# Optimization experiments

Measured on AMD Instinct MI355X. Metric: run time of the kernel, lower is better.

## Reference

```python
import jax, jax.numpy as jnp
import numpy as np


def setup_inputs() -> dict:
    key = jax.random.key(0)
    k1, k2, k3 = jax.random.split(key, 3)
    x = jax.random.normal(k1, (8, 3, 256, 256), dtype=jnp.float32)
    conv_w = jax.random.normal(k2, (64, 3), dtype=jnp.float32)  # 1x1 conv weight [O, C]
    w = jax.random.normal(k3, (64, 8), dtype=jnp.float32)       # per-channel LBP weights
    return {"x": x, "conv_w": conv_w, "w": w}


def _heaviside(d):
    # torch.heaviside(d, 0.): 1 where d > 0, else 0 (including d == 0)
    return jnp.where(d > 0, jnp.ones((), d.dtype), jnp.zeros((), d.dtype))


def reference(x, conv_w, w):
    # 1x1 conv, no bias: [N,C,H,W] x [O,C] -> [N,O,H,W]
    y = jnp.einsum('nchw,oc->nohw', x, conv_w)
    c = y[:, :, 1:-1, 1:-1]  # center, [N,O,H-2,W-2]
    # 8 neighbor shifts in the original order
    shifts = [
        y[:, :, 0:-2, 0:-2], y[:, :, 0:-2, 1:-1], y[:, :, 0:-2, 2:],
        y[:, :, 1:-1, 0:-2], y[:, :, 2:, 0:-2], y[:, :, 2:, 1:-1],
        y[:, :, 2:, 2:],    y[:, :, 1:-1, 2:],
    ]
    act = jnp.stack([_heaviside(c - s) for s in shifts], axis=2)  # [N,O,8,H-2,W-2]
    # weighted reduction over the 8 directions with exp(w)
    x_cat = jnp.einsum('nolhw,ol->nohw', act, jnp.exp(w))
    padded = jnp.pad(x_cat, ((0, 0), (0, 0), (1, 1), (1, 1)))  # ZeroPad2d(1)
    # res=True: concat raw input along channels -> [N, 3+O, H, W]
    return jnp.concatenate([x, padded], axis=1)
```

## Files before the change

### kernel.cpp

```cpp
#include <hip/hip_runtime.h>


__device__ __forceinline__ float wave_shr1(float v) {
    return __int_as_float(
        __builtin_amdgcn_update_dpp(0, __float_as_int(v), 0x138, 0xf, 0xf, false));
}
__device__ __forceinline__ float wave_shl1(float v) {
    return __int_as_float(
        __builtin_amdgcn_update_dpp(0, __float_as_int(v), 0x130, 0xf, 0xf, false));
}

__global__ __launch_bounds__(256) void lbp_all(
    const float* __restrict__ x,
    const float* __restrict__ conv_w,
    const float* __restrict__ w,
    float* __restrict__ out)
{
#pragma clang fp contract(off)
    const int n    = blockIdx.z;
    const int og   = blockIdx.y;
    const int tid  = threadIdx.x;
    const int lane = tid & 63;
    const int wv   = tid >> 6;
    const int col  = lane * 4;
    const int R    = blockIdx.x * 8;
    const int hrow0 = R + wv * 2;

    __shared__ float xt[3][10][256];
    __shared__ float ews[128];

    if (tid < 128) ews[tid] = expf(w[og * 128 + tid]);

    const float* xn = x + (size_t)n * 3 * 65536;

    for (int f = tid; f < 1920; f += 256) {
        const int ch = f / 640;
        const int rr = (f - ch * 640) >> 6;
        const int l4 = f & 63;
        int gr = R - 1 + rr;
        gr = gr < 0 ? 0 : (gr > 255 ? 255 : gr);
        *(float4*)&xt[ch][rr][l4 * 4] =
            *(const float4*)(xn + (size_t)ch * 65536 + (size_t)gr * 256 + l4 * 4);
    }
    __syncthreads();

    if (og == 0) {
        #pragma unroll
        for (int ch = 0; ch < 3; ++ch) {
            float* cp = out + ((((size_t)n * 67 + ch) * 256 + hrow0) * 256 + col);
            *(float4*)cp         = *(const float4*)&xt[ch][2 * wv + 1][col];
            *(float4*)(cp + 256) = *(const float4*)&xt[ch][2 * wv + 2][col];
        }
    }

    float* obase = out + ((((size_t)n * 67 + 3 + og * 16) * 256 + hrow0) * 256 + col);

    #pragma unroll 1
    for (int oi = 0; oi < 16; ++oi) {
        const int o = og * 16 + oi;
        const float cw0 = conv_w[o * 3 + 0];
        const float cw1 = conv_w[o * 3 + 1];
        const float cw2 = conv_w[o * 3 + 2];

        const float e0 = ews[oi * 8 + 0], e1 = ews[oi * 8 + 1];
        const float e2 = ews[oi * 8 + 2], e3 = ews[oi * 8 + 3];
        const float e4 = ews[oi * 8 + 4], e5 = ews[oi * 8 + 5];
        const float e6 = ews[oi * 8 + 6], e7 = ews[oi * 8 + 7];

        float Y[4][6];
        #pragma unroll
        for (int r = 0; r < 4; ++r) {
            const int lr = 2 * wv + r;
            const float4 a = *(const float4*)&xt[0][lr][col];
            const float4 b = *(const float4*)&xt[1][lr][col];
            const float4 c = *(const float4*)&xt[2][lr][col];
            float4 yv;
            yv.x = a.x * cw0 + b.x * cw1 + c.x * cw2;
            yv.y = a.y * cw0 + b.y * cw1 + c.y * cw2;
            yv.z = a.z * cw0 + b.z * cw1 + c.z * cw2;
            yv.w = a.w * cw0 + b.w * cw1 + c.w * cw2;
            Y[r][1] = yv.x; Y[r][2] = yv.y; Y[r][3] = yv.z; Y[r][4] = yv.w;
            Y[r][0] = wave_shr1(yv.w);
            Y[r][5] = wave_shl1(yv.x);
        }

        #pragma unroll
        for (int k = 0; k < 2; ++k) {
            const int hrow = hrow0 + k;
            float res[4];
            if (hrow == 0 || hrow == 255) {
                res[0] = res[1] = res[2] = res[3] = 0.f;
            } else {
                const float* up  = Y[k];
                const float* mid = Y[k + 1];
                const float* dn  = Y[k + 2];
                #pragma unroll
                for (int j = 0; j < 4; ++j) {
                    const float c = mid[j + 1];
                    const float n0 = (c > up [j    ]) ? e0 : 0.f;
                    const float n1 = (c > up [j + 1]) ? e1 : 0.f;
                    const float n2 = (c > up [j + 2]) ? e2 : 0.f;
                    const float n3 = (c > mid[j    ]) ? e3 : 0.f;
                    const float n4 = (c > dn [j    ]) ? e4 : 0.f;
                    const float n5 = (c > dn [j + 1]) ? e5 : 0.f;
                    const float n6 = (c > dn [j + 2]) ? e6 : 0.f;
                    const float n7 = (c > mid[j + 2]) ? e7 : 0.f;
                    res[j] = ((n0 + n1) + (n2 + n3)) + ((n4 + n5) + (n6 + n7));
                }
                if (lane == 0)  res[0] = 0.f;
                if (lane == 63) res[3] = 0.f;
            }
            *(float4*)(obase + (size_t)oi * 65536 + (size_t)k * 256) =
                make_float4(res[0], res[1], res[2], res[3]);
        }
    }
}

extern "C" void kernel_launch(void* const* d_in, const int* in_sizes, int n_in,
                              void* d_out, int out_size, void* d_ws, size_t ws_size,
                              hipStream_t stream) {
    const float* x      = (const float*)d_in[0];
    const float* conv_w = (const float*)d_in[1];
    const float* w      = (const float*)d_in[2];
    float* out          = (float*)d_out;

    dim3 grid(32, 4, 8);
    dim3 block(256);
    hipLaunchKernelGGL(lbp_all, grid, block, 0, stream, x, conv_w, w, out);
}
```

Baseline: 154.2 us.

## Assign one output channel per wave and stream rows through a rolling register window

Work is remapped so each wave owns one output channel over a 16-row strip, instead of looping over 16 channels for 2 rows. The 1x1 conv result is kept in a rotating 4-row register window, so only one new row is computed per output row. This cuts the redundant conv recomputation from halo rows and moves the exp(w) weights into per-wave scalar registers. Blocks become 1024 threads with a taller shared tile, which may lower occupancy. The 8-term sum is now accumulated sequentially rather than as a tree, which changes float rounding slightly.

```diff
diff --git a/kernel.cpp b/kernel.cpp
--- a/kernel.cpp
+++ b/kernel.cpp
@@ -10,7 +10,7 @@
         __builtin_amdgcn_update_dpp(0, __float_as_int(v), 0x130, 0xf, 0xf, false));
 }
 
-__global__ __launch_bounds__(256) void lbp_all(
+__global__ __launch_bounds__(1024) void lbp_all(
     const float* __restrict__ x,
     const float* __restrict__ conv_w,
     const float* __restrict__ w,
@@ -23,97 +23,104 @@
     const int lane = tid & 63;
     const int wv   = tid >> 6;
     const int col  = lane * 4;
-    const int R    = blockIdx.x * 8;
-    const int hrow0 = R + wv * 2;
+    const int s    = blockIdx.x * 16;
+    const int c    = og * 16 + wv;
 
-    __shared__ float xt[3][10][256];
-    __shared__ float ews[128];
-
-    if (tid < 128) ews[tid] = expf(w[og * 128 + tid]);
+    __shared__ float xt[3][18][256];
 
     const float* xn = x + (size_t)n * 3 * 65536;
 
-    for (int f = tid; f < 1920; f += 256) {
-        const int ch = f / 640;
-        const int rr = (f - ch * 640) >> 6;
-        const int l4 = f & 63;
-        int gr = R - 1 + rr;
+    for (int f = tid; f < 3456; f += 1024) {
+        const int ch  = f / 1152;
+        const int rem = f - ch * 1152;
+        const int rr  = rem >> 6;
+        const int l4  = rem & 63;
+        int gr = s - 1 + rr;
         gr = gr < 0 ? 0 : (gr > 255 ? 255 : gr);
         *(float4*)&xt[ch][rr][l4 * 4] =
             *(const float4*)(xn + (size_t)ch * 65536 + (size_t)gr * 256 + l4 * 4);
     }
+
+    const float cw0 = conv_w[c * 3 + 0];
+    const float cw1 = conv_w[c * 3 + 1];
+    const float cw2 = conv_w[c * 3 + 2];
+    float ee[8];
+    #pragma unroll
+    for (int i = 0; i < 8; ++i)
+        ee[i] = __uint_as_float(__builtin_amdgcn_readfirstlane(
+                    __float_as_uint(expf(w[c * 8 + i]))));
+    const float e0 = ee[0], e1 = ee[1], e2 = ee[2], e3 = ee[3];
+    const float e4 = ee[4], e5 = ee[5], e6 = ee[6], e7 = ee[7];
+
     __syncthreads();
 
-    if (og == 0) {
-        #pragma unroll
-        for (int ch = 0; ch < 3; ++ch) {
-            float* cp = out + ((((size_t)n * 67 + ch) * 256 + hrow0) * 256 + col);
-            *(float4*)cp         = *(const float4*)&xt[ch][2 * wv + 1][col];
-            *(float4*)(cp + 256) = *(const float4*)&xt[ch][2 * wv + 2][col];
-        }
+    if (og == 0 && wv < 3) {
+        float* cp = out + ((((size_t)n * 67 + wv) * 256 + s) * 256 + col);
+        #pragma unroll 4
+        for (int r = 0; r < 16; ++r)
+            *(float4*)(cp + (size_t)r * 256) = *(const float4*)&xt[wv][r + 1][col];
     }
 
-    float* obase = out + ((((size_t)n * 67 + 3 + og * 16) * 256 + hrow0) * 256 + col);
+    float* ob = out + ((((size_t)n * 67 + 3 + c) * 256 + s) * 256 + col);
 
-    #pragma unroll 1
-    for (int oi = 0; oi < 16; ++oi) {
-        const int o = og * 16 + oi;
-        const float cw0 = conv_w[o * 3 + 0];
-        const float cw1 = conv_w[o * 3 + 1];
-        const float cw2 = conv_w[o * 3 + 2];
+    float Y[4][6];
 
-        const float e0 = ews[oi * 8 + 0], e1 = ews[oi * 8 + 1];
-        const float e2 = ews[oi * 8 + 2], e3 = ews[oi * 8 + 3];
-        const float e4 = ews[oi * 8 + 4], e5 = ews[oi * 8 + 5];
-        const float e6 = ews[oi * 8 + 6], e7 = ews[oi * 8 + 7];
+#define CONV(SLOT, IDX) do {                                                  \
+        const float4 a  = *(const float4*)&xt[0][(IDX)][col];                 \
+        const float4 b  = *(const float4*)&xt[1][(IDX)][col];                 \
+        const float4 cc = *(const float4*)&xt[2][(IDX)][col];                 \
+        float4 yv;                                                            \
+        yv.x = a.x * cw0 + b.x * cw1 + cc.x * cw2;                            \
+        yv.y = a.y * cw0 + b.y * cw1 + cc.y * cw2;                            \
+        yv.z = a.z * cw0 + b.z * cw1 + cc.z * cw2;                            \
+        yv.w = a.w * cw0 + b.w * cw1 + cc.w * cw2;                            \
+        Y[SLOT][1] = yv.x; Y[SLOT][2] = yv.y;                                 \
+        Y[SLOT][3] = yv.z; Y[SLOT][4] = yv.w;                                 \
+        Y[SLOT][0] = wave_shr1(yv.w);                                         \
+        Y[SLOT][5] = wave_shl1(yv.x);                                         \
+    } while (0)
 
-        float Y[4][6];
-        #pragma unroll
-        for (int r = 0; r < 4; ++r) {
-            const int lr = 2 * wv + r;
-            const float4 a = *(const float4*)&xt[0][lr][col];
-            const float4 b = *(const float4*)&xt[1][lr][col];
-            const float4 c = *(const float4*)&xt[2][lr][col];
-            float4 yv;
-            yv.x = a.x * cw0 + b.x * cw1 + c.x * cw2;
-            yv.y = a.y * cw0 + b.y * cw1 + c.y * cw2;
-            yv.z = a.z * cw0 + b.z * cw1 + c.z * cw2;
-            yv.w = a.w * cw0 + b.w * cw1 + c.w * cw2;
-            Y[r][1] = yv.x; Y[r][2] = yv.y; Y[r][3] = yv.z; Y[r][4] = yv.w;
-            Y[r][0] = wave_shr1(yv.w);
-            Y[r][5] = wave_shl1(yv.x);
-        }
+    CONV(3, 0);
+    CONV(0, 1);
 
-        #pragma unroll
-        for (int k = 0; k < 2; ++k) {
-            const int hrow = hrow0 + k;
-            float res[4];
-            if (hrow == 0 || hrow == 255) {
-                res[0] = res[1] = res[2] = res[3] = 0.f;
-            } else {
-                const float* up  = Y[k];
-                const float* mid = Y[k + 1];
-                const float* dn  = Y[k + 2];
-                #pragma unroll
-                for (int j = 0; j < 4; ++j) {
-                    const float c = mid[j + 1];
-                    const float n0 = (c > up [j    ]) ? e0 : 0.f;
-                    const float n1 = (c > up [j + 1]) ? e1 : 0.f;
-                    const float n2 = (c > up [j + 2]) ? e2 : 0.f;
-                    const float n3 = (c > mid[j    ]) ? e3 : 0.f;
-                    const float n4 = (c > dn [j    ]) ? e4 : 0.f;
-                    const float n5 = (c > dn [j + 1]) ? e5 : 0.f;
-                    const float n6 = (c > dn [j + 2]) ? e6 : 0.f;
-                    const float n7 = (c > mid[j + 2]) ? e7 : 0.f;
-                    res[j] = ((n0 + n1) + (n2 + n3)) + ((n4 + n5) + (n6 + n7));
-                }
-                if (lane == 0)  res[0] = 0.f;
-                if (lane == 63) res[3] = 0.f;
-            }
-            *(float4*)(obase + (size_t)oi * 65536 + (size_t)k * 256) =
-                make_float4(res[0], res[1], res[2], res[3]);
-        }
+#define STEP(JI) do {                                                         \
+    const int j = jq + (JI);                                                  \
+    const int r = s + j;                                                      \
+    CONV(((JI) + 1) & 3, j + 2);                                  \
+    const float* up  = Y[((JI) + 3) & 3];                         \
+    const float* mid = Y[(JI) & 3];                               \
+    const float* dn  = Y[((JI) + 1) & 3];                         \
+    float res[4];                                                             \
+    if (r == 0 || r == 255) {                               \
+        res[0] = res[1] = res[2] = res[3] = 0.f;                              \
+    } else {                                                                  \
+        _Pragma("unroll")                                                     \
+        for (int jj = 0; jj < 4; ++jj) {                                      \
+            const float cv = mid[jj + 1];                                     \
+            float acc;                                                        \
+            acc  = (cv > up [jj    ]) ? e0 : 0.f;                \
+            acc += (cv > up [jj + 1]) ? e1 : 0.f;                \
+            acc += (cv > up [jj + 2]) ? e2 : 0.f;                \
+            acc += (cv > mid[jj    ]) ? e3 : 0.f;                \
+            acc += (cv > dn [jj    ]) ? e4 : 0.f;                \
+            acc += (cv > dn [jj + 1]) ? e5 : 0.f;                \
+            acc += (cv > dn [jj + 2]) ? e6 : 0.f;                \
+            acc += (cv > mid[jj + 2]) ? e7 : 0.f;                \
+            res[jj] = acc;                                                    \
+        }                                                                     \
+        if (lane == 0)  res[0] = 0.f;                            \
+        if (lane == 63) res[3] = 0.f;                            \
+    }                                                                         \
+    *(float4*)(ob + (size_t)j * 256) =                                        \
+        make_float4(res[0], res[1], res[2], res[3]);                          \
+} while (0)
+
+    #pragma unroll
+    for (int jq = 0; jq < 16; jq += 4) {
+        STEP(0); STEP(1); STEP(2); STEP(3);
     }
+#undef STEP
+#undef CONV
 }
 
 extern "C" void kernel_launch(void* const* d_in, const int* in_sizes, int n_in,
@@ -124,7 +131,7 @@
     const float* w      = (const float*)d_in[2];
     float* out          = (float*)d_out;
 
-    dim3 grid(32, 4, 8);
-    dim3 block(256);
+    dim3 grid(16, 4, 8);
+    dim3 block(1024);
     hipLaunchKernelGGL(lbp_all, grid, block, 0, stream, x, conv_w, w, out);
 }
```

Measured after the change: 156.0 us. About the same (+1.2%).
